# Optimization experiments

Hardware: AMD Instinct MI355X
Metric: run time of the kernel (lower is better)

## Reference

```python
import jax, jax.numpy as jnp
import numpy as np

N, E, F, C, K, N_G, N_M = 100000, 600000, 6, 128, 3, 2, 2


def setup_inputs() -> dict:
    key = jax.random.key(0)
    ks = jax.random.split(key, 12)
    x = jax.random.normal(ks[0], (N, F), dtype=jnp.float32)
    edge_index = jax.random.randint(ks[1], (2, E), 0, N, dtype=jnp.int32)
    s = 0.05
    W0 = jax.random.normal(ks[2], (F, C), dtype=jnp.float32) * s
    b0 = jnp.zeros((C,), dtype=jnp.float32)
    # TAGConv: per layer, K+1 hop weights (no per-lin bias) + one shared bias
    W_tag = jax.random.normal(ks[3], (N_G, K + 1, C, C), dtype=jnp.float32) * s
    b_tag = jnp.zeros((N_G, C), dtype=jnp.float32)
    W_mlp = jax.random.normal(ks[4], (N_M, C, C), dtype=jnp.float32) * s
    b_mlp = jnp.zeros((N_M, C), dtype=jnp.float32)
    W1 = jax.random.normal(ks[5], (C, 1), dtype=jnp.float32) * s
    b1 = jnp.zeros((1,), dtype=jnp.float32)
    return {"x": x, "edge_index": edge_index, "W0": W0, "b0": b0,
            "W_tag": W_tag, "b_tag": b_tag, "W_mlp": W_mlp, "b_mlp": b_mlp,
            "W1": W1, "b1": b1}


def reference(x, edge_index, W0, b0, W_tag, b_tag, W_mlp, b_mlp, W1, b1):
    row, col = edge_index[0], edge_index[1]  # source -> target
    n = x.shape[0]
    # GCN-style symmetric normalization, no self-loops (PyG TAGConv default)
    deg = jax.ops.segment_sum(jnp.ones((row.shape[0],), x.dtype), col, num_segments=n)
    dis = jnp.where(deg > 0, jax.lax.rsqrt(jnp.maximum(deg, 1.0)), 0.0)
    norm = dis[row] * dis[col]  # [E]

    h = jax.nn.relu(x @ W0 + b0)  # lin0

    for g in range(W_tag.shape[0]):  # n_G TAGConv layers
        out = h @ W_tag[g, 0]
        xk = h
        for k in range(1, W_tag.shape[1]):  # K hops
            msg = norm[:, None] * xk[row]           # [E, C] gather
            xk = jax.ops.segment_sum(msg, col, num_segments=n)  # scatter-add
            out = out + xk @ W_tag[g, k]
        h = jax.nn.relu(out + b_tag[g])

    for m in range(W_mlp.shape[0]):  # mlp block
        h = jax.nn.relu(h @ W_mlp[m] + b_mlp[m])

    return jax.nn.relu(h @ W1 + b1)  # [N, 1]
```

## Files before the change

### kernel.cpp

```cpp
#include <hip/hip_runtime.h>

#define NN 100000
#define NP 100096
#define NE 600000
#define CC 128

typedef __attribute__((ext_vector_type(4))) float f32x4;
typedef _Float16 h8 __attribute__((ext_vector_type(8)));
typedef _Float16 h2 __attribute__((ext_vector_type(2)));


__global__ void k_deg(const int* __restrict__ col, int* __restrict__ deg) {
  int e = blockIdx.x * 256 + threadIdx.x;
  if (e < NE) atomicAdd(&deg[col[e]], 1);
}

__global__ void k_dis(const int* __restrict__ deg, float* __restrict__ dis) {
  int n = blockIdx.x * 256 + threadIdx.x;
  if (n >= NP) return;
  int d = (n < NN) ? deg[n] : 0;
  dis[n] = (d > 0) ? rsqrtf((float)d) : 0.0f;
}

__global__ void k_scan1(const int* __restrict__ deg, int* __restrict__ rowptr,
                        int* __restrict__ bsum) {
  __shared__ int s[1024];
  int t = threadIdx.x;
  int i = blockIdx.x * 1024 + t;
  int v = (i < NN) ? deg[i] : 0;
  s[t] = v;
  __syncthreads();
  #pragma unroll
  for (int off = 1; off < 1024; off <<= 1) {
    int tv = (t >= off) ? s[t - off] : 0;
    __syncthreads();
    s[t] += tv;
    __syncthreads();
  }
  if (i < NN) rowptr[i] = s[t] - v;
  if (t == 1023) bsum[blockIdx.x] = s[1023];
}

__global__ void k_scan2(const int* __restrict__ bsum, int* __restrict__ bsum2) {
  __shared__ int s[128];
  int t = threadIdx.x;
  int v = (t < 98) ? bsum[t] : 0;
  s[t] = v;
  __syncthreads();
  #pragma unroll
  for (int off = 1; off < 128; off <<= 1) {
    int tv = (t >= off) ? s[t - off] : 0;
    __syncthreads();
    s[t] += tv;
    __syncthreads();
  }
  bsum2[t] = s[t] - v;
}

__global__ void k_scan3(int* __restrict__ rowptr, const int* __restrict__ bsum2) {
  int i = blockIdx.x * 1024 + threadIdx.x;
  if (i < NN) rowptr[i] += bsum2[blockIdx.x];
}

__global__ void k_rptail(int* __restrict__ rowptr) {
  int i = NN + blockIdx.x * 256 + threadIdx.x;
  if (i < NP + 8) rowptr[i] = NE;
}

__global__ void k_fill(const int* __restrict__ row, const int* __restrict__ col,
                       const float* __restrict__ dis, const int* __restrict__ rowptr,
                       int* __restrict__ cnt, int2* __restrict__ csr) {
  int e = blockIdx.x * 256 + threadIdx.x;
  if (e >= NE) return;
  int c = col[e], r = row[e];
  int pos = rowptr[c] + atomicAdd(&cnt[c], 1);
  int2 v;
  v.x = r * CC;
  v.y = __float_as_int(dis[r] * dis[c]);
  csr[pos] = v;
}


__global__ void k_lin0(const float* __restrict__ x, const float* __restrict__ W0,
                       const float* __restrict__ b0, _Float16* __restrict__ h) {
  int idx = blockIdx.x * 256 + threadIdx.x;
  int n = idx >> 7, c = idx & 127;
  if (n >= NP) return;
  float v = 0.0f;
  if (n < NN) {
    v = b0[c];
    #pragma unroll
    for (int f = 0; f < 6; ++f) v = fmaf(x[n * 6 + f], W0[f * CC + c], v);
    v = fmaxf(v, 0.0f);
  }
  h[idx] = (_Float16)v;
}


__global__ void k_wconv(const float* __restrict__ src, _Float16* __restrict__ dst, int K) {
  int tid = blockIdx.x * 256 + threadIdx.x;
  if (tid >= K * 128) return;
  int e = tid & 7, l = (tid >> 3) & 63, nb = (tid >> 9) & 7, kb = tid >> 12;
  int k = kb * 32 + (l >> 4) * 8 + e;
  int c = nb * 16 + (l & 15);
  dst[tid] = (_Float16)src[k * 128 + c];
}


__global__ __launch_bounds__(256) void k_prop(const int* __restrict__ rowptr,
                                              const int2* __restrict__ csr,
                                              const _Float16* __restrict__ xin,
                                              _Float16* __restrict__ xout) {
  int gid = blockIdx.x * 256 + threadIdx.x;
  int wv = gid >> 6;
  int lane = gid & 63;
  int n0 = wv * 4;
  if (n0 >= NP) return;
  int b0 = rowptr[n0], b1 = rowptr[n0 + 1], b2 = rowptr[n0 + 2],
      b3 = rowptr[n0 + 3], b4 = rowptr[n0 + 4];
  int e4 = b4 - b0;

  int2 ew; ew.x = 0; ew.y = 0;
  int gl = 0;
  if (lane < e4) {
    int pos = b0 + lane;
    ew = csr[pos];
    gl = (pos >= b1) + (pos >= b2) + (pos >= b3);
  }

  float a00 = 0, a01 = 0, a10 = 0, a11 = 0, a20 = 0, a21 = 0, a30 = 0, a31 = 0;
  int nb = e4 < 64 ? e4 : 64;
  for (int j = 0; j < nb; j += 8) {
    #pragma unroll
    for (int u = 0; u < 8; ++u) {
      int off = __shfl(ew.x, j + u);
      float w = __uint_as_float(__shfl(ew.y, j + u));
      int gg = __shfl(gl, j + u);
      h2 v = *reinterpret_cast<const h2*>(&xin[off + lane * 2]);
      float v0 = (float)v[0], v1 = (float)v[1];
      float w0 = (gg == 0) ? w : 0.0f;
      float w1 = (gg == 1) ? w : 0.0f;
      float w2 = (gg == 2) ? w : 0.0f;
      float w3 = (gg == 3) ? w : 0.0f;
      a00 += w0 * v0; a01 += w0 * v1;
      a10 += w1 * v0; a11 += w1 * v1;
      a20 += w2 * v0; a21 += w2 * v1;
      a30 += w3 * v0; a31 += w3 * v1;
    }
  }
  for (int j = 64; j < e4; ++j) {
    int pos = b0 + j;
    int2 e2 = csr[pos];
    float w = __uint_as_float(e2.y);
    int gg = (pos >= b1) + (pos >= b2) + (pos >= b3);
    h2 v = *reinterpret_cast<const h2*>(&xin[e2.x + lane * 2]);
    float v0 = (float)v[0], v1 = (float)v[1];
    float w0 = (gg == 0) ? w : 0.0f;
    float w1 = (gg == 1) ? w : 0.0f;
    float w2 = (gg == 2) ? w : 0.0f;
    float w3 = (gg == 3) ? w : 0.0f;
    a00 += w0 * v0; a01 += w0 * v1;
    a10 += w1 * v0; a11 += w1 * v1;
    a20 += w2 * v0; a21 += w2 * v1;
    a30 += w3 * v0; a31 += w3 * v1;
  }

  h2 o;
  o[0] = (_Float16)a00; o[1] = (_Float16)a01;
  *reinterpret_cast<h2*>(&xout[(size_t)(n0 + 0) * CC + lane * 2]) = o;
  o[0] = (_Float16)a10; o[1] = (_Float16)a11;
  *reinterpret_cast<h2*>(&xout[(size_t)(n0 + 1) * CC + lane * 2]) = o;
  o[0] = (_Float16)a20; o[1] = (_Float16)a21;
  *reinterpret_cast<h2*>(&xout[(size_t)(n0 + 2) * CC + lane * 2]) = o;
  o[0] = (_Float16)a30; o[1] = (_Float16)a31;
  *reinterpret_cast<h2*>(&xout[(size_t)(n0 + 3) * CC + lane * 2]) = o;
}


template<int KB, bool BR>
__global__ __launch_bounds__(256) void k_mm(const _Float16* __restrict__ X0,
                                            const _Float16* __restrict__ X1,
                                            const _Float16* __restrict__ X2,
                                            const _Float16* __restrict__ X3,
                                            const _Float16* __restrict__ Wp,
                                            const float* __restrict__ bias,
                                            _Float16* __restrict__ Y) {
  __shared__ _Float16 lds[128 * 128];
  int t = threadIdx.x;
  int w = t >> 6, l = t & 63;
  int lr = l & 15, lk = l >> 4;
  int m0w = (w & 1) * 64;
  int nb0 = (w >> 1) * 4;
  long row0 = (long)blockIdx.x * 128;
  const _Float16* Xs[4] = {X0, X1, X2, X3};

  f32x4 acc[4][4];
  #pragma unroll
  for (int m = 0; m < 4; ++m)
    #pragma unroll
    for (int n = 0; n < 4; ++n) acc[m][n] = (f32x4){0.f, 0.f, 0.f, 0.f};

  #pragma unroll
  for (int xi = 0; xi < KB; ++xi) {
    const _Float16* __restrict__ xb = Xs[xi];
    #pragma unroll
    for (int i = 0; i < 8; ++i) {
      int li = i * 256 + t;
      int r = li >> 4, ck = li & 15;
      int cs = ck ^ (r & 7);
      const _Float16* src = xb + (size_t)(row0 + r) * CC + cs * 8;
      _Float16* dst = lds + ((size_t)i * 2048 + (size_t)(t & 192) * 8);
      __builtin_amdgcn_global_load_lds((const __attribute__((address_space(1))) void*)src,
                                       (__attribute__((address_space(3))) void*)dst,
                                       16, 0, 0);
    }
    __syncthreads();

    #pragma unroll
    for (int kk = 0; kk < 4; ++kk) {
      int kb = xi * 4 + kk;
      h8 a[4], b[4];
      #pragma unroll
      for (int m = 0; m < 4; ++m) {
        int R = m0w + m * 16 + lr;
        a[m] = *reinterpret_cast<const h8*>(&lds[R * 128 + (((kk * 4 + lk) ^ (lr & 7)) << 3)]);
      }
      #pragma unroll
      for (int n = 0; n < 4; ++n)
        b[n] = *reinterpret_cast<const h8*>(&Wp[((size_t)(kb * 8 + nb0 + n) * 64 + l) * 8]);
      #pragma unroll
      for (int m = 0; m < 4; ++m)
        #pragma unroll
        for (int n = 0; n < 4; ++n)
          acc[m][n] = __builtin_amdgcn_mfma_f32_16x16x32_f16(a[m], b[n], acc[m][n], 0, 0, 0);
    }
    __syncthreads();
  }

  int r0 = m0w + lk * 4;
  long rb = row0 + r0;
  #pragma unroll
  for (int m = 0; m < 4; ++m) {
    #pragma unroll
    for (int n = 0; n < 4; ++n) {
      int c = (nb0 + n) * 16 + lr;
      float bv = BR ? bias[c] : 0.0f;
      #pragma unroll
      for (int q = 0; q < 4; ++q) {
        float v = acc[m][n][q] + bv;
        if (BR) v = fmaxf(v, 0.0f);
        Y[(rb + m * 16 + q) * CC + c] = (_Float16)v;
      }
    }
  }
}


__global__ void k_head(const _Float16* __restrict__ h, const float* __restrict__ W1,
                       const float* __restrict__ b1, float* __restrict__ out) {
  int gid = blockIdx.x * 256 + threadIdx.x;
  int wid = gid >> 6, lane = gid & 63;
  if (wid >= NN) return;
  const _Float16* hp = &h[wid * CC];
  float v = (float)hp[lane] * W1[lane] + (float)hp[lane + 64] * W1[lane + 64];
  #pragma unroll
  for (int o = 32; o > 0; o >>= 1) v += __shfl_down(v, o);
  if (lane == 0) out[wid] = fmaxf(v + b1[0], 0.0f);
}


extern "C" void kernel_launch(void* const* d_in, const int* in_sizes, int n_in,
                              void* d_out, int out_size, void* d_ws, size_t ws_size,
                              hipStream_t stream) {
  const float* x     = (const float*)d_in[0];
  const int*   ei    = (const int*)d_in[1];
  const float* W0    = (const float*)d_in[2];
  const float* b0    = (const float*)d_in[3];
  const float* W_tag = (const float*)d_in[4];
  const float* b_tag = (const float*)d_in[5];
  const float* W_mlp = (const float*)d_in[6];
  const float* b_mlp = (const float*)d_in[7];
  const float* W1    = (const float*)d_in[8];
  const float* b1    = (const float*)d_in[9];
  const int* row = ei;
  const int* col = ei + NE;

  char* p = (char*)d_ws;
  auto carve = [&](size_t bytes) { void* r = (void*)p; p += (bytes + 255) & ~(size_t)255; return r; };
  _Float16* hA   = (_Float16*)carve((size_t)NP * CC * 2);
  _Float16* hB   = (_Float16*)carve((size_t)NP * CC * 2);
  _Float16* x1   = (_Float16*)carve((size_t)NP * CC * 2);
  _Float16* x2   = (_Float16*)carve((size_t)NP * CC * 2);
  _Float16* x3   = (_Float16*)carve((size_t)NP * CC * 2);
  _Float16* WpT0 = (_Float16*)carve((size_t)512 * CC * 2);
  _Float16* WpT1 = (_Float16*)carve((size_t)512 * CC * 2);
  _Float16* WpM0 = (_Float16*)carve((size_t)CC * CC * 2);
  _Float16* WpM1 = (_Float16*)carve((size_t)CC * CC * 2);
  float* dis     = (float*)carve((size_t)NP * 4);
  int*   deg     = (int*)carve((size_t)NP * 4);
  int*   rowptr  = (int*)carve((size_t)(NP + 8) * 4);
  int*   cnt     = (int*)carve((size_t)NN * 4);
  int*   bsum    = (int*)carve(512);
  int*   bsum2   = (int*)carve(512);
  int2*  csr     = (int2*)carve((size_t)NE * 8);

  hipMemsetAsync(deg, 0, (size_t)NP * 4, stream);
  hipMemsetAsync(cnt, 0, (size_t)NN * 4, stream);

  k_deg<<<(NE + 255) / 256, 256, 0, stream>>>(col, deg);
  k_dis<<<(NP + 255) / 256, 256, 0, stream>>>(deg, dis);
  k_scan1<<<98, 1024, 0, stream>>>(deg, rowptr, bsum);
  k_scan2<<<1, 128, 0, stream>>>(bsum, bsum2);
  k_scan3<<<98, 1024, 0, stream>>>(rowptr, bsum2);
  k_rptail<<<1, 256, 0, stream>>>(rowptr);
  k_fill<<<(NE + 255) / 256, 256, 0, stream>>>(row, col, dis, rowptr, cnt, csr);

  k_wconv<<<(512 * CC + 255) / 256, 256, 0, stream>>>(W_tag,            WpT0, 512);
  k_wconv<<<(512 * CC + 255) / 256, 256, 0, stream>>>(W_tag + 512 * CC, WpT1, 512);
  k_wconv<<<(CC * CC + 255) / 256, 256, 0, stream>>>(W_mlp,             WpM0, 128);
  k_wconv<<<(CC * CC + 255) / 256, 256, 0, stream>>>(W_mlp + CC * CC,   WpM1, 128);

  k_lin0<<<NP * CC / 256, 256, 0, stream>>>(x, W0, b0, hA);

  const int GB = NP / 128;
  const int PB = (NP / 4) * 64 / 256;

  _Float16* hc = hA;
  _Float16* hn = hB;
  const _Float16* WpT[2] = {WpT0, WpT1};
  for (int g = 0; g < 2; ++g) {
    k_prop<<<PB, 256, 0, stream>>>(rowptr, csr, hc, x1);
    k_prop<<<PB, 256, 0, stream>>>(rowptr, csr, x1, x2);
    k_prop<<<PB, 256, 0, stream>>>(rowptr, csr, x2, x3);
    k_mm<4, true><<<GB, 256, 0, stream>>>(hc, x1, x2, x3, WpT[g], b_tag + (size_t)g * CC, hn);
    _Float16* tmp = hc; hc = hn; hn = tmp;
  }

  k_mm<1, true><<<GB, 256, 0, stream>>>(hc, nullptr, nullptr, nullptr, WpM0, b_mlp, hn);
  { _Float16* tmp = hc; hc = hn; hn = tmp; }
  k_mm<1, true><<<GB, 256, 0, stream>>>(hc, nullptr, nullptr, nullptr, WpM1, b_mlp + CC, hn);
  { _Float16* tmp = hc; hc = hn; hn = tmp; }

  k_head<<<(NN * 64) / 256, 256, 0, stream>>>(hc, W1, b1, (float*)d_out);
}
```

Measured before the change: 402.1 us.

## Double-buffer GEMM LDS staging, prefetch gathers in prop, merge setup launches

```diff
diff --git a/kernel.cpp b/kernel.cpp
--- a/kernel.cpp
+++ b/kernel.cpp
@@ -41,9 +41,11 @@
   if (t == 1023) bsum[blockIdx.x] = s[1023];
 }
 
-__global__ void k_scan2(const int* __restrict__ bsum, int* __restrict__ bsum2) {
+__global__ void k_scan2(const int* __restrict__ bsum, int* __restrict__ bsum2,
+                        int* __restrict__ rowptr) {
+  int t = threadIdx.x;
+  if (t < NP + 8 - NN) rowptr[NN + t] = NE;
   __shared__ int s[128];
-  int t = threadIdx.x;
   int v = (t < 98) ? bsum[t] : 0;
   s[t] = v;
   __syncthreads();
@@ -60,11 +62,6 @@
 __global__ void k_scan3(int* __restrict__ rowptr, const int* __restrict__ bsum2) {
   int i = blockIdx.x * 1024 + threadIdx.x;
   if (i < NN) rowptr[i] += bsum2[blockIdx.x];
-}
-
-__global__ void k_rptail(int* __restrict__ rowptr) {
-  int i = NN + blockIdx.x * 256 + threadIdx.x;
-  if (i < NP + 8) rowptr[i] = NE;
 }
 
 __global__ void k_fill(const int* __restrict__ row, const int* __restrict__ col,
@@ -130,22 +127,44 @@
 
   float a00 = 0, a01 = 0, a10 = 0, a11 = 0, a20 = 0, a21 = 0, a30 = 0, a31 = 0;
   int nb = e4 < 64 ? e4 : 64;
-  for (int j = 0; j < nb; j += 8) {
+
+  if (nb > 0) {
+    h2 vb[8]; float wb[8]; int gb[8];
     #pragma unroll
     for (int u = 0; u < 8; ++u) {
-      int off = __shfl(ew.x, j + u);
-      float w = __uint_as_float(__shfl(ew.y, j + u));
-      int gg = __shfl(gl, j + u);
-      h2 v = *reinterpret_cast<const h2*>(&xin[off + lane * 2]);
-      float v0 = (float)v[0], v1 = (float)v[1];
-      float w0 = (gg == 0) ? w : 0.0f;
-      float w1 = (gg == 1) ? w : 0.0f;
-      float w2 = (gg == 2) ? w : 0.0f;
-      float w3 = (gg == 3) ? w : 0.0f;
-      a00 += w0 * v0; a01 += w0 * v1;
-      a10 += w1 * v0; a11 += w1 * v1;
-      a20 += w2 * v0; a21 += w2 * v1;
-      a30 += w3 * v0; a31 += w3 * v1;
+      int off = __shfl(ew.x, u);
+      wb[u] = __uint_as_float(__shfl(ew.y, u));
+      gb[u] = __shfl(gl, u);
+      vb[u] = *reinterpret_cast<const h2*>(&xin[off + lane * 2]);
+    }
+    for (int j = 0; j < nb; j += 8) {
+      h2 vn[8]; float wn[8]; int gn[8];
+      #pragma unroll
+      for (int u = 0; u < 8; ++u) { vn[u] = vb[u]; wn[u] = 0.0f; gn[u] = 0; }
+      if (j + 8 < nb) {
+        #pragma unroll
+        for (int u = 0; u < 8; ++u) {
+          int off = __shfl(ew.x, j + 8 + u);
+          wn[u] = __uint_as_float(__shfl(ew.y, j + 8 + u));
+          gn[u] = __shfl(gl, j + 8 + u);
+          vn[u] = *reinterpret_cast<const h2*>(&xin[off + lane * 2]);
+        }
+      }
+      #pragma unroll
+      for (int u = 0; u < 8; ++u) {
+        float v0 = (float)vb[u][0], v1 = (float)vb[u][1];
+        float w = wb[u]; int gg = gb[u];
+        float w0 = (gg == 0) ? w : 0.0f;
+        float w1 = (gg == 1) ? w : 0.0f;
+        float w2 = (gg == 2) ? w : 0.0f;
+        float w3 = (gg == 3) ? w : 0.0f;
+        a00 += w0 * v0; a01 += w0 * v1;
+        a10 += w1 * v0; a11 += w1 * v1;
+        a20 += w2 * v0; a21 += w2 * v1;
+        a30 += w3 * v0; a31 += w3 * v1;
+      }
+      #pragma unroll
+      for (int u = 0; u < 8; ++u) { vb[u] = vn[u]; wb[u] = wn[u]; gb[u] = gn[u]; }
     }
   }
   for (int j = 64; j < e4; ++j) {
@@ -185,7 +204,7 @@
                                             const _Float16* __restrict__ Wp,
                                             const float* __restrict__ bias,
                                             _Float16* __restrict__ Y) {
-  __shared__ _Float16 lds[128 * 128];
+  __shared__ _Float16 lds[2][128 * 128];
   int t = threadIdx.x;
   int w = t >> 6, l = t & 63;
   int lr = l & 15, lk = l >> 4;
@@ -194,27 +213,38 @@
   long row0 = (long)blockIdx.x * 128;
   const _Float16* Xs[4] = {X0, X1, X2, X3};
 
-  f32x4 acc[4][4];
-  #pragma unroll
-  for (int m = 0; m < 4; ++m)
-    #pragma unroll
-    for (int n = 0; n < 4; ++n) acc[m][n] = (f32x4){0.f, 0.f, 0.f, 0.f};
-
-  #pragma unroll
-  for (int xi = 0; xi < KB; ++xi) {
-    const _Float16* __restrict__ xb = Xs[xi];
+  auto stage = [&](int buf, const _Float16* __restrict__ xb) {
     #pragma unroll
     for (int i = 0; i < 8; ++i) {
       int li = i * 256 + t;
       int r = li >> 4, ck = li & 15;
       int cs = ck ^ (r & 7);
       const _Float16* src = xb + (size_t)(row0 + r) * CC + cs * 8;
-      _Float16* dst = lds + ((size_t)i * 2048 + (size_t)(t & 192) * 8);
+      _Float16* dst = &lds[buf][i * 2048 + (t & 192) * 8];
       __builtin_amdgcn_global_load_lds((const __attribute__((address_space(1))) void*)src,
                                        (__attribute__((address_space(3))) void*)dst,
                                        16, 0, 0);
     }
-    __syncthreads();
+  };
+
+  f32x4 acc[4][4];
+  #pragma unroll
+  for (int m = 0; m < 4; ++m)
+    #pragma unroll
+    for (int n = 0; n < 4; ++n) acc[m][n] = (f32x4){0.f, 0.f, 0.f, 0.f};
+
+  stage(0, Xs[0]);
+  #pragma unroll
+  for (int xi = 0; xi < KB; ++xi) {
+    if (xi + 1 < KB) {
+      stage((xi + 1) & 1, Xs[xi + 1]);
+      asm volatile("s_waitcnt vmcnt(8)" ::: "memory");
+    } else {
+      asm volatile("s_waitcnt vmcnt(0)" ::: "memory");
+    }
+    __builtin_amdgcn_sched_barrier(0);
+    __builtin_amdgcn_s_barrier();
+    const _Float16* __restrict__ lb = lds[xi & 1];
 
     #pragma unroll
     for (int kk = 0; kk < 4; ++kk) {
@@ -223,7 +253,7 @@
       #pragma unroll
       for (int m = 0; m < 4; ++m) {
         int R = m0w + m * 16 + lr;
-        a[m] = *reinterpret_cast<const h8*>(&lds[R * 128 + (((kk * 4 + lk) ^ (lr & 7)) << 3)]);
+        a[m] = *reinterpret_cast<const h8*>(&lb[R * 128 + (((kk * 4 + lk) ^ (lr & 7)) << 3)]);
       }
       #pragma unroll
       for (int n = 0; n < 4; ++n)
@@ -234,7 +264,7 @@
         for (int n = 0; n < 4; ++n)
           acc[m][n] = __builtin_amdgcn_mfma_f32_16x16x32_f16(a[m], b[n], acc[m][n], 0, 0, 0);
     }
-    __syncthreads();
+    __builtin_amdgcn_s_barrier();
   }
 
   int r0 = m0w + lk * 4;
@@ -261,7 +291,7 @@
   int gid = blockIdx.x * 256 + threadIdx.x;
   int wid = gid >> 6, lane = gid & 63;
   if (wid >= NN) return;
-  const _Float16* hp = &h[wid * CC];
+  const _Float16* hp = &h[(size_t)wid * CC];
   float v = (float)hp[lane] * W1[lane] + (float)hp[lane + 64] * W1[lane + 64];
   #pragma unroll
   for (int o = 32; o > 0; o >>= 1) v += __shfl_down(v, o);
@@ -292,33 +322,28 @@
   _Float16* x1   = (_Float16*)carve((size_t)NP * CC * 2);
   _Float16* x2   = (_Float16*)carve((size_t)NP * CC * 2);
   _Float16* x3   = (_Float16*)carve((size_t)NP * CC * 2);
-  _Float16* WpT0 = (_Float16*)carve((size_t)512 * CC * 2);
-  _Float16* WpT1 = (_Float16*)carve((size_t)512 * CC * 2);
-  _Float16* WpM0 = (_Float16*)carve((size_t)CC * CC * 2);
-  _Float16* WpM1 = (_Float16*)carve((size_t)CC * CC * 2);
+  _Float16* WpT  = (_Float16*)carve((size_t)1024 * CC * 2);
+  _Float16* WpM  = (_Float16*)carve((size_t)256 * CC * 2);
   float* dis     = (float*)carve((size_t)NP * 4);
-  int*   deg     = (int*)carve((size_t)NP * 4);
+  int*   dc      = (int*)carve((size_t)(NP + NN) * 4);
+  int*   deg     = dc;
+  int*   cnt     = dc + NP;
   int*   rowptr  = (int*)carve((size_t)(NP + 8) * 4);
-  int*   cnt     = (int*)carve((size_t)NN * 4);
   int*   bsum    = (int*)carve(512);
   int*   bsum2   = (int*)carve(512);
   int2*  csr     = (int2*)carve((size_t)NE * 8);
 
-  hipMemsetAsync(deg, 0, (size_t)NP * 4, stream);
-  hipMemsetAsync(cnt, 0, (size_t)NN * 4, stream);
+  hipMemsetAsync(dc, 0, (size_t)(NP + NN) * 4, stream);
 
   k_deg<<<(NE + 255) / 256, 256, 0, stream>>>(col, deg);
   k_dis<<<(NP + 255) / 256, 256, 0, stream>>>(deg, dis);
   k_scan1<<<98, 1024, 0, stream>>>(deg, rowptr, bsum);
-  k_scan2<<<1, 128, 0, stream>>>(bsum, bsum2);
+  k_scan2<<<1, 128, 0, stream>>>(bsum, bsum2, rowptr);
   k_scan3<<<98, 1024, 0, stream>>>(rowptr, bsum2);
-  k_rptail<<<1, 256, 0, stream>>>(rowptr);
   k_fill<<<(NE + 255) / 256, 256, 0, stream>>>(row, col, dis, rowptr, cnt, csr);
 
-  k_wconv<<<(512 * CC + 255) / 256, 256, 0, stream>>>(W_tag,            WpT0, 512);
-  k_wconv<<<(512 * CC + 255) / 256, 256, 0, stream>>>(W_tag + 512 * CC, WpT1, 512);
-  k_wconv<<<(CC * CC + 255) / 256, 256, 0, stream>>>(W_mlp,             WpM0, 128);
-  k_wconv<<<(CC * CC + 255) / 256, 256, 0, stream>>>(W_mlp + CC * CC,   WpM1, 128);
+  k_wconv<<<(1024 * CC + 255) / 256, 256, 0, stream>>>(W_tag, WpT, 1024);
+  k_wconv<<<(256 * CC + 255) / 256, 256, 0, stream>>>(W_mlp, WpM, 256);
 
   k_lin0<<<NP * CC / 256, 256, 0, stream>>>(x, W0, b0, hA);
 
@@ -327,19 +352,17 @@
 
   _Float16* hc = hA;
   _Float16* hn = hB;
-  const _Float16* WpT[2] = {WpT0, WpT1};
   for (int g = 0; g < 2; ++g) {
     k_prop<<<PB, 256, 0, stream>>>(rowptr, csr, hc, x1);
     k_prop<<<PB, 256, 0, stream>>>(rowptr, csr, x1, x2);
     k_prop<<<PB, 256, 0, stream>>>(rowptr, csr, x2, x3);
-    k_mm<4, true><<<GB, 256, 0, stream>>>(hc, x1, x2, x3, WpT[g], b_tag + (size_t)g * CC, hn);
+    k_mm<4, true><<<GB, 256, 0, stream>>>(hc, x1, x2, x3, WpT + (size_t)g * 512 * CC,
+                                          b_tag + (size_t)g * CC, hn);
     _Float16* tmp = hc; hc = hn; hn = tmp;
   }
 
-  k_mm<1, true><<<GB, 256, 0, stream>>>(hc, nullptr, nullptr, nullptr, WpM0, b_mlp, hn);
-  { _Float16* tmp = hc; hc = hn; hn = tmp; }
-  k_mm<1, true><<<GB, 256, 0, stream>>>(hc, nullptr, nullptr, nullptr, WpM1, b_mlp + CC, hn);
-  { _Float16* tmp = hc; hc = hn; hn = tmp; }
-
-  k_head<<<(NN * 64) / 256, 256, 0, stream>>>(hc, W1, b1, (float*)d_out);
-}
+  k_mm<1, true><<<GB, 256, 0, stream>>>(hc, nullptr, nullptr, nullptr, WpM, b_mlp, x1);
+  k_mm<1, true><<<GB, 256, 0, stream>>>(x1, nullptr, nullptr, nullptr, WpM + CC * CC,
+                                        b_mlp + CC, x2);
+  k_head<<<(NN * 64) / 256, 256, 0, stream>>>(x2, W1, b1, (float*)d_out);
+}
```

Measured after the change: 415.7 us. 1.03x slower.
